# Performance work log

Hardware: AMD Instinct MI355X
Metric: run time of the kernel (lower is better)

The kernel has to match this reference:

```python
import jax, jax.numpy as jnp
import numpy as np

LN_EPS = 1e-5

def _layernorm(x, g, b):
    mu = jnp.mean(x, axis=-1, keepdims=True)
    var = jnp.var(x, axis=-1, keepdims=True)
    return (x - mu) * jax.lax.rsqrt(var + LN_EPS) * g + b

def setup_inputs() -> dict:
    key = jax.random.key(0)
    ks = jax.random.split(key, 8)
    B, L, d_atom, d_hid = 8, 128, 256, 32
    return {
        "z":    jax.random.normal(ks[0], (B, L, d_atom), dtype=jnp.float32),
        "W_in": jax.random.normal(ks[1], (d_atom, 2 * d_hid), dtype=jnp.float32) * 0.02,
        "b_in": jnp.zeros((2 * d_hid,), dtype=jnp.float32),
        "ln_g": jnp.ones((2 * d_hid,), dtype=jnp.float32),
        "ln_b": jnp.zeros((2 * d_hid,), dtype=jnp.float32),
        "W1":   jax.random.normal(ks[2], (d_hid * d_hid, 21), dtype=jnp.float32) * 0.02,
        "b1":   jnp.zeros((21,), dtype=jnp.float32),
        "W2":   jax.random.normal(ks[3], (d_hid * d_hid, 30), dtype=jnp.float32) * 0.02,
        "b2":   jnp.zeros((30,), dtype=jnp.float32),
    }

def reference(z, W_in, b_in, ln_g, ln_b, W1, b1, W2, b2):
    # linear_in: Linear -> exact GELU -> LayerNorm
    ab = _layernorm(jax.nn.gelu(z @ W_in + b_in, approximate=False), ln_g, ln_b)
    h = ab.shape[-1] // 2
    a, b = ab[..., :h], ab[..., h:]              # (B, L, h) each
    # Fused bilinear form: outer(a_l, b_m) flattened to h*h, then Linear.
    # Equivalent to materializing (B, L, L, h*h) and matmul, reassociated.
    W1r = W1.reshape(h, h, -1)                   # (h, h, 21)
    W2r = W2.reshape(h, h, -1)                   # (h, h, 30)
    x1 = jnp.einsum('blc,bmd,cdk->blmk', a, b, W1r) + b1  # (B, L, L, 21)
    x2 = jnp.einsum('blc,bmd,cdk->blmk', a, b, W2r) + b2  # (B, L, L, 30)
    return (x1, x2)
```

## Files before the change

kernel.cpp:

```cpp
#include <hip/hip_runtime.h>
#include <hip/hip_bf16.h>
#include <math.h>

#define NB 8
#define NL 128
#define D_ATOM 256
#define DH 32
#define DAB 64
#define K1 21
#define K2 30
#define KT 51
#define ROWS (NB*NL)
#define LN_EPS 1e-5f

#define OUT1_ROW (NL*K1)
#define OUT2_ROW (NL*K2)
#define STAGE_N  (OUT1_ROW + OUT2_ROW)
#define WCAT 1632

typedef __attribute__((ext_vector_type(8))) short bf16x8;
typedef __attribute__((ext_vector_type(4))) float f32x4;

__device__ __forceinline__ unsigned short f2bf(float x) {
    __hip_bfloat16 h = __float2bfloat16(x);
    return *reinterpret_cast<unsigned short*>(&h);
}

__global__ __launch_bounds__(256) void ln_wprep_kernel(
    const float* __restrict__ z, const float* __restrict__ W_in,
    const float* __restrict__ b_in, const float* __restrict__ ln_g,
    const float* __restrict__ ln_b, const float* __restrict__ W1,
    const float* __restrict__ W2, float* __restrict__ a_ws,
    unsigned short* __restrict__ bbf, unsigned short* __restrict__ Wlin2)
{
    __shared__ float zT[D_ATOM][2];
    __shared__ float red[16][2][DAB];

    const int t = threadIdx.x;
    const int w = t >> 6, l = t & 63;
    const int g = l >> 4, c4 = l & 15;
    const int row0 = blockIdx.x * 2;

    if (t < 128) {
        const int r = t >> 6, i0 = (t & 63) * 4;
        float4 v = ((const float4*)(z + (size_t)(row0 + r) * D_ATOM))[t & 63];
        zT[i0 + 0][r] = v.x; zT[i0 + 1][r] = v.y;
        zT[i0 + 2][r] = v.z; zT[i0 + 3][r] = v.w;
    }
    __syncthreads();

    float acc[2][4];
    #pragma unroll
    for (int r = 0; r < 2; ++r)
        #pragma unroll
        for (int q = 0; q < 4; ++q) acc[r][q] = 0.f;

    const int ibase = w * 64 + g * 16;
    #pragma unroll
    for (int it = 0; it < 16; ++it) {
        const int i = ibase + it;
        float4 wv = *(const float4*)&W_in[i * DAB + 4 * c4];
        float2 zv = *(const float2*)&zT[i][0];
        float wq[4] = {wv.x, wv.y, wv.z, wv.w};
        #pragma unroll
        for (int q = 0; q < 4; ++q) {
            acc[0][q] = fmaf(zv.x, wq[q], acc[0][q]);
            acc[1][q] = fmaf(zv.y, wq[q], acc[1][q]);
        }
    }
    const int p = w * 4 + g;
    #pragma unroll
    for (int r = 0; r < 2; ++r) {
        float4 v = {acc[r][0], acc[r][1], acc[r][2], acc[r][3]};
        *(float4*)&red[p][r][4 * c4] = v;
    }
    __syncthreads();

    if (t < 128) {
        const int r = t >> 6, j = t & 63;
        float a2 = b_in[j];
        #pragma unroll
        for (int pp = 0; pp < 16; ++pp) a2 += red[pp][r][j];

        float gg = 0.5f * a2 * (1.0f + erff(a2 * 0.70710678118654752f));

        float s = gg, sq = gg * gg;
        #pragma unroll
        for (int msk = 1; msk < 64; msk <<= 1) {
            s  += __shfl_xor(s,  msk, 64);
            sq += __shfl_xor(sq, msk, 64);
        }
        float mu  = s  * (1.0f / 64.0f);
        float var = sq * (1.0f / 64.0f) - mu * mu;
        float y = (gg - mu) * rsqrtf(var + LN_EPS) * ln_g[j] + ln_b[j];

        const int row = row0 + r;
        if (j < DH) {
            a_ws[row * DH + j] = y;
        } else {
            const int d = j - DH, m = row & 127, batch = row >> 7;
            bbf[batch * 4096 + ((m >> 4) << 9) +
                ((((m & 15) | ((d >> 3) << 4)) << 3) | (d & 7))] = f2bf(y);
        }
    }

    if (t < 16) {
        int pw = (int)blockIdx.x * 16 + t;
        int c  = pw >> 8, t2 = pw & 255;
        unsigned short v[8];
        #pragma unroll
        for (int s2 = 0; s2 < 8; ++s2) {
            int o = s2 * 256 + t2;
            float val = 0.f;
            if (o < 672)       val = W1[c * 672 + o];
            else if (o < WCAT) val = W2[c * 960 + (o - 672)];
            v[s2] = f2bf(val);
        }
        uint4 wq;
        wq.x = (unsigned)v[0] | ((unsigned)v[1] << 16);
        wq.y = (unsigned)v[2] | ((unsigned)v[3] << 16);
        wq.z = (unsigned)v[4] | ((unsigned)v[5] << 16);
        wq.w = (unsigned)v[6] | ((unsigned)v[7] << 16);
        ((uint4*)Wlin2)[pw] = wq;
    }
}

__global__ __launch_bounds__(256, 4) void pair_kernel(
    const float* __restrict__ a_ws, const unsigned short* __restrict__ bbf,
    const unsigned short* __restrict__ Wlin2, const float* __restrict__ b1v,
    const float* __restrict__ b2v, float* __restrict__ out)
{
    const int row0  = blockIdx.x * 2;
    const int batch = row0 >> 7;
    const int t     = threadIdx.x;
    const int w  = t >> 6, l = t & 63;
    const int lg = l >> 4, li = l & 15;

    __shared__ unsigned short Tf[2 * 4 * 64 * 8];
    __shared__ __align__(16) float stg[STAGE_N];
    __shared__ float al[2][DH];

    #pragma unroll
    for (int s = 0; s < 8; ++s)
        ((unsigned int*)Tf)[t + s * 256] = 0u;
    if (t < 2 * DH) al[t >> 5][t & 31] = a_ws[row0 * DH + t];
    __syncthreads();

    {
        float tacc0[7], tacc1[7];
        int fidx[7];
        bool val[7];
        #pragma unroll
        for (int s = 0; s < 7; ++s) {
            int o = t + s * 256;
            val[s] = (o < WCAT);
            int oo = val[s] ? o : 0;
            int d, k;
            if (oo < 672) { d = oo / 21; k = oo % 21; }
            else { int o2 = oo - 672; d = o2 / 30; k = 21 + o2 % 30; }
            fidx[s] = (((k >> 4) * 64 + ((k & 15) | ((d >> 3) << 4))) << 3) | (d & 7);
            tacc0[s] = 0.f; tacc1[s] = 0.f;
        }
        const uint4* wbase = ((const uint4*)Wlin2) + t;
        #pragma unroll 4
        for (int c = 0; c < DH; ++c) {
            float ac0 = al[0][c], ac1 = al[1][c];
            uint4 wq = wbase[c * 256];
            float wv[7];
            wv[0] = __uint_as_float(wq.x << 16);
            wv[1] = __uint_as_float(wq.x & 0xffff0000u);
            wv[2] = __uint_as_float(wq.y << 16);
            wv[3] = __uint_as_float(wq.y & 0xffff0000u);
            wv[4] = __uint_as_float(wq.z << 16);
            wv[5] = __uint_as_float(wq.z & 0xffff0000u);
            wv[6] = __uint_as_float(wq.w << 16);
            #pragma unroll
            for (int s = 0; s < 7; ++s) {
                tacc0[s] = fmaf(ac0, wv[s], tacc0[s]);
                tacc1[s] = fmaf(ac1, wv[s], tacc1[s]);
            }
        }
        #pragma unroll
        for (int s = 0; s < 7; ++s) {
            if (val[s]) {
                Tf[fidx[s]]        = f2bf(tacc0[s]);
                Tf[2048 + fidx[s]] = f2bf(tacc1[s]);
            }
        }
    }
    __syncthreads();

    const int r  = w >> 1;
    const int mh = w & 1;

    bf16x8 afr[4], bfr[4];
    #pragma unroll
    for (int i = 0; i < 4; ++i)
        afr[i] = ((const bf16x8*)bbf)[batch * 512 + (mh * 4 + i) * 64 + l];
    #pragma unroll
    for (int kt = 0; kt < 4; ++kt)
        bfr[kt] = ((const bf16x8*)Tf)[(r * 4 + kt) * 64 + l];

    float bias[4];
    #pragma unroll
    for (int kt = 0; kt < 4; ++kt) {
        int k = kt * 16 + li;
        bias[kt] = (k < K1) ? b1v[k] : (k < KT ? b2v[k - K1] : 0.f);
    }

    #pragma unroll
    for (int rr = 0; rr < 2; ++rr) {
        if (r == rr) {
            #pragma unroll
            for (int i = 0; i < 4; ++i) {
                const int mbase = (mh * 4 + i) * 16 + lg * 4;
                #pragma unroll
                for (int kt = 0; kt < 4; ++kt) {
                    f32x4 acc = __builtin_amdgcn_mfma_f32_16x16x32_bf16(
                        afr[i], bfr[kt], (f32x4){0.f, 0.f, 0.f, 0.f}, 0, 0, 0);
                    const int k = kt * 16 + li;
                    if (k < K1) {
                        #pragma unroll
                        for (int q = 0; q < 4; ++q)
                            stg[(mbase + q) * K1 + k] = acc[q] + bias[kt];
                    } else if (k < KT) {
                        #pragma unroll
                        for (int q = 0; q < 4; ++q)
                            stg[OUT1_ROW + (mbase + q) * K2 + (k - K1)] = acc[q] + bias[kt];
                    }
                }
            }
        }
        __syncthreads();

        const int row = row0 + rr;
        float* o1 = out + (size_t)row * OUT1_ROW;
        float* o2 = out + (size_t)ROWS * OUT1_ROW + (size_t)row * OUT2_ROW;
        const float4* s1 = (const float4*)stg;
        const float4* s2 = (const float4*)(stg + OUT1_ROW);
        for (int i4 = t; i4 < OUT1_ROW / 4; i4 += 256)
            ((float4*)o1)[i4] = s1[i4];
        for (int i4 = t; i4 < OUT2_ROW / 4; i4 += 256)
            ((float4*)o2)[i4] = s2[i4];
        if (rr == 0) __syncthreads();
    }
}

extern "C" void kernel_launch(void* const* d_in, const int* in_sizes, int n_in,
                              void* d_out, int out_size, void* d_ws, size_t ws_size,
                              hipStream_t stream) {
    const float* z    = (const float*)d_in[0];
    const float* W_in = (const float*)d_in[1];
    const float* b_in = (const float*)d_in[2];
    const float* ln_g = (const float*)d_in[3];
    const float* ln_b = (const float*)d_in[4];
    const float* W1   = (const float*)d_in[5];
    const float* b1   = (const float*)d_in[6];
    const float* W2   = (const float*)d_in[7];
    const float* b2   = (const float*)d_in[8];
    float* out = (float*)d_out;

    float*          a_ws  = (float*)d_ws;
    unsigned short* bbf   = (unsigned short*)(a_ws + 32768);
    unsigned short* Wlin2 = bbf + 32768;

    ln_wprep_kernel<<<ROWS / 2, 256, 0, stream>>>(z, W_in, b_in, ln_g, ln_b,
                                                  W1, W2, a_ws, bbf, Wlin2);
    pair_kernel<<<ROWS / 2, 256, 0, stream>>>(a_ws, bbf, Wlin2, b1, b2, out);
}
```

Before: 21.38 us.

## Move per-row T contraction into LN kernel and pass T via workspace

The per-row contraction of the layernormed 'a' vector with W1/W2 now runs in the first kernel, reading fp32 weights directly, instead of the pair kernel using a bf16 pre-packed weight copy. The result T is staged in LDS and written to global workspace in MFMA fragment layout, so the pair kernel only loads fragments and zero-masks unused lanes. This shortens the pair kernel's prologue and drops its LDS T buffer, at the cost of strided uncoalesced fp32 weight reads in the first kernel and an extra global round trip for T.

```diff
diff --git a/kernel.cpp b/kernel.cpp
--- a/kernel.cpp
+++ b/kernel.cpp
@@ -16,7 +16,7 @@
 #define OUT1_ROW (NL*K1)
 #define OUT2_ROW (NL*K2)
 #define STAGE_N  (OUT1_ROW + OUT2_ROW)
-#define WCAT 1632
+#define TROW_HW 2048
 
 typedef __attribute__((ext_vector_type(8))) short bf16x8;
 typedef __attribute__((ext_vector_type(4))) float f32x4;
@@ -26,15 +26,17 @@
     return *reinterpret_cast<unsigned short*>(&h);
 }
 
-__global__ __launch_bounds__(256) void ln_wprep_kernel(
+__global__ __launch_bounds__(256) void ln_t_kernel(
     const float* __restrict__ z, const float* __restrict__ W_in,
     const float* __restrict__ b_in, const float* __restrict__ ln_g,
     const float* __restrict__ ln_b, const float* __restrict__ W1,
-    const float* __restrict__ W2, float* __restrict__ a_ws,
-    unsigned short* __restrict__ bbf, unsigned short* __restrict__ Wlin2)
+    const float* __restrict__ W2, unsigned short* __restrict__ bbf,
+    unsigned short* __restrict__ T_ws)
 {
     __shared__ float zT[D_ATOM][2];
     __shared__ float red[16][2][DAB];
+    __shared__ float al[2][DH];
+    __shared__ unsigned short Tst[2 * TROW_HW];
 
     const int t = threadIdx.x;
     const int w = t >> 6, l = t & 63;
@@ -96,102 +98,77 @@
 
         const int row = row0 + r;
         if (j < DH) {
-            a_ws[row * DH + j] = y;
+            al[r][j] = y;
         } else {
             const int d = j - DH, m = row & 127, batch = row >> 7;
             bbf[batch * 4096 + ((m >> 4) << 9) +
                 ((((m & 15) | ((d >> 3) << 4)) << 3) | (d & 7))] = f2bf(y);
         }
     }
-
-    if (t < 16) {
-        int pw = (int)blockIdx.x * 16 + t;
-        int c  = pw >> 8, t2 = pw & 255;
-        unsigned short v[8];
-        #pragma unroll
-        for (int s2 = 0; s2 < 8; ++s2) {
-            int o = s2 * 256 + t2;
-            float val = 0.f;
-            if (o < 672)       val = W1[c * 672 + o];
-            else if (o < WCAT) val = W2[c * 960 + (o - 672)];
-            v[s2] = f2bf(val);
-        }
-        uint4 wq;
-        wq.x = (unsigned)v[0] | ((unsigned)v[1] << 16);
-        wq.y = (unsigned)v[2] | ((unsigned)v[3] << 16);
-        wq.z = (unsigned)v[4] | ((unsigned)v[5] << 16);
-        wq.w = (unsigned)v[6] | ((unsigned)v[7] << 16);
-        ((uint4*)Wlin2)[pw] = wq;
-    }
+    __syncthreads();
+
+    {
+        float tacc0[7], tacc1[7];
+        const float* wptr[7];
+        int wstr[7], fidx[7];
+        bool val[7];
+        #pragma unroll
+        for (int s = 0; s < 7; ++s) {
+            int o = t + s * 256;
+            val[s] = (o < 1632);
+            int oo = val[s] ? o : 0;
+            int d, k;
+            if (oo < 672) {
+                wptr[s] = W1 + oo; wstr[s] = 672;
+                d = oo / 21; k = oo % 21;
+            } else {
+                int o2 = oo - 672;
+                wptr[s] = W2 + o2; wstr[s] = 960;
+                d = o2 / 30; k = 21 + o2 % 30;
+            }
+            fidx[s] = (((k >> 4) * 64 + ((k & 15) | ((d >> 3) << 4))) << 3) | (d & 7);
+            tacc0[s] = 0.f; tacc1[s] = 0.f;
+        }
+        #pragma unroll 4
+        for (int c = 0; c < DH; ++c) {
+            float ac0 = al[0][c], ac1 = al[1][c];
+            #pragma unroll
+            for (int s = 0; s < 7; ++s) {
+                float wv = wptr[s][c * wstr[s]];
+                tacc0[s] = fmaf(ac0, wv, tacc0[s]);
+                tacc1[s] = fmaf(ac1, wv, tacc1[s]);
+            }
+        }
+        #pragma unroll
+        for (int s = 0; s < 7; ++s) {
+            if (val[s]) {
+                Tst[fidx[s]]           = f2bf(tacc0[s]);
+                Tst[TROW_HW + fidx[s]] = f2bf(tacc1[s]);
+            }
+        }
+    }
+    __syncthreads();
+
+    uint4* dst = (uint4*)(T_ws + (size_t)row0 * TROW_HW);
+    const uint4* src = (const uint4*)Tst;
+    dst[t]       = src[t];
+    dst[t + 256] = src[t + 256];
 }
 
 __global__ __launch_bounds__(256, 4) void pair_kernel(
-    const float* __restrict__ a_ws, const unsigned short* __restrict__ bbf,
-    const unsigned short* __restrict__ Wlin2, const float* __restrict__ b1v,
-    const float* __restrict__ b2v, float* __restrict__ out)
+    const unsigned short* __restrict__ bbf, const unsigned short* __restrict__ T_ws,
+    const float* __restrict__ b1v, const float* __restrict__ b2v,
+    float* __restrict__ out)
 {
     const int row0  = blockIdx.x * 2;
     const int batch = row0 >> 7;
     const int t     = threadIdx.x;
-    const int w  = t >> 6, l = t & 63;
+    const int w = t >> 6, l = t & 63;
     const int lg = l >> 4, li = l & 15;
-
-    __shared__ unsigned short Tf[2 * 4 * 64 * 8];
+    const int r = w >> 1;
+    const int mh = w & 1;
+
     __shared__ __align__(16) float stg[STAGE_N];
-    __shared__ float al[2][DH];
-
-    #pragma unroll
-    for (int s = 0; s < 8; ++s)
-        ((unsigned int*)Tf)[t + s * 256] = 0u;
-    if (t < 2 * DH) al[t >> 5][t & 31] = a_ws[row0 * DH + t];
-    __syncthreads();
-
-    {
-        float tacc0[7], tacc1[7];
-        int fidx[7];
-        bool val[7];
-        #pragma unroll
-        for (int s = 0; s < 7; ++s) {
-            int o = t + s * 256;
-            val[s] = (o < WCAT);
-            int oo = val[s] ? o : 0;
-            int d, k;
-            if (oo < 672) { d = oo / 21; k = oo % 21; }
-            else { int o2 = oo - 672; d = o2 / 30; k = 21 + o2 % 30; }
-            fidx[s] = (((k >> 4) * 64 + ((k & 15) | ((d >> 3) << 4))) << 3) | (d & 7);
-            tacc0[s] = 0.f; tacc1[s] = 0.f;
-        }
-        const uint4* wbase = ((const uint4*)Wlin2) + t;
-        #pragma unroll 4
-        for (int c = 0; c < DH; ++c) {
-            float ac0 = al[0][c], ac1 = al[1][c];
-            uint4 wq = wbase[c * 256];
-            float wv[7];
-            wv[0] = __uint_as_float(wq.x << 16);
-            wv[1] = __uint_as_float(wq.x & 0xffff0000u);
-            wv[2] = __uint_as_float(wq.y << 16);
-            wv[3] = __uint_as_float(wq.y & 0xffff0000u);
-            wv[4] = __uint_as_float(wq.z << 16);
-            wv[5] = __uint_as_float(wq.z & 0xffff0000u);
-            wv[6] = __uint_as_float(wq.w << 16);
-            #pragma unroll
-            for (int s = 0; s < 7; ++s) {
-                tacc0[s] = fmaf(ac0, wv[s], tacc0[s]);
-                tacc1[s] = fmaf(ac1, wv[s], tacc1[s]);
-            }
-        }
-        #pragma unroll
-        for (int s = 0; s < 7; ++s) {
-            if (val[s]) {
-                Tf[fidx[s]]        = f2bf(tacc0[s]);
-                Tf[2048 + fidx[s]] = f2bf(tacc1[s]);
-            }
-        }
-    }
-    __syncthreads();
-
-    const int r  = w >> 1;
-    const int mh = w & 1;
 
     bf16x8 afr[4], bfr[4];
     #pragma unroll
@@ -199,7 +176,12 @@
         afr[i] = ((const bf16x8*)bbf)[batch * 512 + (mh * 4 + i) * 64 + l];
     #pragma unroll
     for (int kt = 0; kt < 4; ++kt)
-        bfr[kt] = ((const bf16x8*)Tf)[(r * 4 + kt) * 64 + l];
+        bfr[kt] = ((const bf16x8*)T_ws)[(size_t)(row0 + r) * 256 + kt * 64 + l];
+
+    if (li >= 3) {
+        bf16x8 zz = {0, 0, 0, 0, 0, 0, 0, 0};
+        bfr[3] = zz;
+    }
 
     float bias[4];
     #pragma unroll
@@ -260,11 +242,10 @@
     const float* b2   = (const float*)d_in[8];
     float* out = (float*)d_out;
 
-    float*          a_ws  = (float*)d_ws;
-    unsigned short* bbf   = (unsigned short*)(a_ws + 32768);
-    unsigned short* Wlin2 = bbf + 32768;
-
-    ln_wprep_kernel<<<ROWS / 2, 256, 0, stream>>>(z, W_in, b_in, ln_g, ln_b,
-                                                  W1, W2, a_ws, bbf, Wlin2);
-    pair_kernel<<<ROWS / 2, 256, 0, stream>>>(a_ws, bbf, Wlin2, b1, b2, out);
-}
+    unsigned short* bbf  = (unsigned short*)d_ws;
+    unsigned short* T_ws = bbf + 32768;
+
+    ln_t_kernel<<<ROWS / 2, 256, 0, stream>>>(z, W_in, b_in, ln_g, ln_b,
+                                              W1, W2, bbf, T_ws);
+    pair_kernel<<<ROWS / 2, 256, 0, stream>>>(bbf, T_ws, b1, b2, out);
+}
```

New measurement: 23.43 us. 1.1x slower.
